# Optimization experiments

Hardware: AMD Instinct MI355X
Metric: run time of the kernel (lower is better)

The kernel has to match this reference:

```python
import jax, jax.numpy as jnp
import numpy as np

N_RAYS = 131072
N_SAMPLES = 128
FEAT_DIM = 3
FAR_DELTA = 1e10  # sentinel delta appended for the last sample, as in the torch code


def setup_inputs() -> dict:
    key = jax.random.key(0)
    k1, k2, k3 = jax.random.split(key, 3)
    # densities are non-negative (output of e.g. relu/softplus in NeRF)
    density = jax.random.uniform(k1, (N_RAYS, N_SAMPLES), dtype=jnp.float32) * 2.0
    feature = jax.random.uniform(k2, (N_RAYS, N_SAMPLES, FEAT_DIM), dtype=jnp.float32)
    # monotonically increasing per-ray sample depths: near + cumsum(uniform bins)
    bins = jax.random.uniform(k3, (N_RAYS, N_SAMPLES), dtype=jnp.float32) * 0.05 + 0.01
    depth_values = 1.0 + jnp.cumsum(bins, axis=1)
    return {"density": density, "feature": feature, "depth_values": depth_values}


def reference(density, feature, depth_values):
    # deltas: consecutive depth differences, with a huge last delta (torch.cat(..., 1e10*ones))
    deltas = jnp.concatenate(
        [depth_values[:, 1:] - depth_values[:, :-1],
         jnp.full_like(depth_values[:, :1], FAR_DELTA)],
        axis=-1,
    )  # [N, S]
    att = jnp.exp(-density * deltas)              # exp(-sigma_i * delta_i), [N, S]
    # inclusive prefix product, matching the loop: T[i] = T[i-1]*exp(-sigma_i*delta_i)
    T = jnp.cumprod(att, axis=1)                  # [N, S]
    weights = T * (1.0 - att)                     # [N, S]
    feat_out = jnp.einsum("ns,nsc->nc", weights, feature)      # [N, 3]
    depth_out = jnp.sum(weights * depth_values, axis=1)         # [N]
    return feat_out, depth_out
```

## Files before the change

kernel.cpp:

```cpp
#include <hip/hip_runtime.h>

#define N_RAYS    131072
#define N_SAMPLES 128
#define FAR_DELTA 1e10f

#define THREADS_PER_RAY 8
#define SPT (N_SAMPLES / THREADS_PER_RAY)

__global__ __launch_bounds__(256) void VolumeRenderer_57612691308835_kernel(
    const float* __restrict__ density,
    const float* __restrict__ feature,
    const float* __restrict__ depth,
    float* __restrict__ out_feat,
    float* __restrict__ out_depth)
{
    const int gtid = blockIdx.x * 256 + threadIdx.x;
    const int ray  = gtid >> 3;
    const int sub  = gtid & 7;

    const long sbase = (long)ray * N_SAMPLES + sub * SPT;
    const float4* __restrict__ dp4 = (const float4*)(depth   + sbase);
    const float4* __restrict__ dn4 = (const float4*)(density + sbase);
    const float4* __restrict__ ft4 = (const float4*)(feature + sbase * 3);

    float dep[SPT + 1], den[SPT], f[SPT * 3];
    #pragma unroll
    for (int g = 0; g < SPT / 4; ++g) {
        const float4 v = dp4[g];
        dep[4*g+0] = v.x; dep[4*g+1] = v.y; dep[4*g+2] = v.z; dep[4*g+3] = v.w;
    }
    #pragma unroll
    for (int g = 0; g < SPT / 4; ++g) {
        const float4 v = dn4[g];
        den[4*g+0] = v.x; den[4*g+1] = v.y; den[4*g+2] = v.z; den[4*g+3] = v.w;
    }
    #pragma unroll
    for (int g = 0; g < SPT * 3 / 4; ++g) {
        const float4 v = ft4[g];
        f[4*g+0] = v.x; f[4*g+1] = v.y; f[4*g+2] = v.z; f[4*g+3] = v.w;
    }

    dep[SPT] = __shfl_down(dep[0], 1);

    float Tloc = 1.0f;
    float sfx = 0.f, sfy = 0.f, sfz = 0.f, sdd = 0.f;
    #pragma unroll
    for (int i = 0; i < SPT; ++i) {
        const float delta = (sub == 7 && i == SPT - 1) ? FAR_DELTA
                                                       : (dep[i + 1] - dep[i]);
        const float att = __expf(-den[i] * delta);
        Tloc *= att;
        const float w = Tloc * (1.0f - att);
        sfx += w * f[3*i + 0];
        sfy += w * f[3*i + 1];
        sfz += w * f[3*i + 2];
        sdd += w * dep[i];
    }

    float p = Tloc, v;
    v = __shfl_up(p, 1); if (sub >= 1) p *= v;
    v = __shfl_up(p, 2); if (sub >= 2) p *= v;
    v = __shfl_up(p, 4); if (sub >= 4) p *= v;
    float excl = __shfl_up(p, 1);
    if (sub == 0) excl = 1.0f;

    sfx *= excl; sfy *= excl; sfz *= excl; sdd *= excl;

    #pragma unroll
    for (int off = 1; off <= 4; off <<= 1) {
        sfx += __shfl_xor(sfx, off);
        sfy += __shfl_xor(sfy, off);
        sfz += __shfl_xor(sfz, off);
        sdd += __shfl_xor(sdd, off);
    }

    if (sub == 0) {
        out_feat[ray * 3 + 0] = sfx;
        out_feat[ray * 3 + 1] = sfy;
        out_feat[ray * 3 + 2] = sfz;
        out_depth[ray]        = sdd;
    }
}

extern "C" void kernel_launch(void* const* d_in, const int* in_sizes, int n_in,
                              void* d_out, int out_size, void* d_ws, size_t ws_size,
                              hipStream_t stream) {
    const float* density = (const float*)d_in[0];
    const float* feature = (const float*)d_in[1];
    const float* depth   = (const float*)d_in[2];

    float* out_feat  = (float*)d_out;
    float* out_depth = (float*)d_out + (long)N_RAYS * 3;

    const int total_threads = N_RAYS * THREADS_PER_RAY;
    const int grid = total_threads / 256;
    VolumeRenderer_57612691308835_kernel<<<grid, 256, 0, stream>>>(
        density, feature, depth, out_feat, out_depth);
}
```

Baseline: 372.9 us.

## Stage loads through padded LDS for fully coalesced global reads, 16 threads per ray

Each block now loads its rays' density, depth and feature data with fully coalesced float4 reads, where consecutive threads touch consecutive addresses. The data is staged in padded shared memory to avoid bank conflicts, and each thread then reads back its own sample slice. Threads per ray go from 8 to 16, which adds one more step to the shuffle scan and the reduction. The feature data reuses the same LDS buffer in a second phase, so the kernel now needs extra barriers and holds more registers for the prefetched values.

```diff
diff --git a/kernel.cpp b/kernel.cpp
--- a/kernel.cpp
+++ b/kernel.cpp
@@ -4,8 +4,19 @@
 #define N_SAMPLES 128
 #define FAR_DELTA 1e10f
 
-#define THREADS_PER_RAY 8
-#define SPT (N_SAMPLES / THREADS_PER_RAY)
+#define TPB 256
+#define TPR 16
+#define SPT (N_SAMPLES / TPR)
+#define RPB (TPB / TPR)
+
+#define LDS_WORDS (20 * 384 + 16)
+
+__device__ __forceinline__ int lds_addr(int chunk, int j) {
+    return 20 * chunk + j;
+}
+__device__ __forceinline__ int lds_addr_w(int chunk_base, int W) {
+    return lds_addr(chunk_base + (W >> 4), W & 15);
+}
 
 __global__ __launch_bounds__(256) void VolumeRenderer_57612691308835_kernel(
     const float* __restrict__ density,
@@ -14,60 +25,95 @@
     float* __restrict__ out_feat,
     float* __restrict__ out_depth)
 {
-    const int gtid = blockIdx.x * 256 + threadIdx.x;
-    const int ray  = gtid >> 3;
-    const int sub  = gtid & 7;
+    __shared__ float lds[LDS_WORDS];
 
-    const long sbase = (long)ray * N_SAMPLES + sub * SPT;
-    const float4* __restrict__ dp4 = (const float4*)(depth   + sbase);
-    const float4* __restrict__ dn4 = (const float4*)(density + sbase);
-    const float4* __restrict__ ft4 = (const float4*)(feature + sbase * 3);
+    const int tid = threadIdx.x;
+    const int r   = tid >> 4;
+    const int sub = tid & 15;
+    const int blockRay0 = blockIdx.x * RPB;
 
-    float dep[SPT + 1], den[SPT], f[SPT * 3];
+    const float4* gden = (const float4*)(density + (long)blockRay0 * N_SAMPLES);
+    const float4* gdep = (const float4*)(depth   + (long)blockRay0 * N_SAMPLES);
+    const float4* gft  = (const float4*)(feature + (long)blockRay0 * N_SAMPLES * 3);
+    float4 ld_den[2], ld_dep[2], ld_ft[6];
     #pragma unroll
-    for (int g = 0; g < SPT / 4; ++g) {
-        const float4 v = dp4[g];
-        dep[4*g+0] = v.x; dep[4*g+1] = v.y; dep[4*g+2] = v.z; dep[4*g+3] = v.w;
+    for (int s = 0; s < 2; ++s) ld_den[s] = gden[tid + s * 256];
+    #pragma unroll
+    for (int s = 0; s < 2; ++s) ld_dep[s] = gdep[tid + s * 256];
+    #pragma unroll
+    for (int s = 0; s < 6; ++s) ld_ft[s]  = gft[tid + s * 256];
+
+    #pragma unroll
+    for (int s = 0; s < 2; ++s) {
+        const int W = s * 1024 + 4 * tid;
+        *(float4*)&lds[lds_addr_w(0,   W)] = ld_den[s];
+        *(float4*)&lds[lds_addr_w(128, W)] = ld_dep[s];
     }
-    #pragma unroll
-    for (int g = 0; g < SPT / 4; ++g) {
-        const float4 v = dn4[g];
-        den[4*g+0] = v.x; den[4*g+1] = v.y; den[4*g+2] = v.z; den[4*g+3] = v.w;
+    __syncthreads();
+
+    float den[SPT], dep[SPT];
+    {
+        const int cA = 8 * r + (sub >> 1);
+        const int j0 = 8 * (sub & 1);
+        #pragma unroll
+        for (int h = 0; h < 2; ++h) {
+            const float4 v = *(const float4*)&lds[lds_addr(cA,       j0 + 4 * h)];
+            const float4 w = *(const float4*)&lds[lds_addr(128 + cA, j0 + 4 * h)];
+            den[4*h+0] = v.x; den[4*h+1] = v.y; den[4*h+2] = v.z; den[4*h+3] = v.w;
+            dep[4*h+0] = w.x; dep[4*h+1] = w.y; dep[4*h+2] = w.z; dep[4*h+3] = w.w;
+        }
     }
-    #pragma unroll
-    for (int g = 0; g < SPT * 3 / 4; ++g) {
-        const float4 v = ft4[g];
-        f[4*g+0] = v.x; f[4*g+1] = v.y; f[4*g+2] = v.z; f[4*g+3] = v.w;
-    }
+    const float next_dep = __shfl_down(dep[0], 1);
 
-    dep[SPT] = __shfl_down(dep[0], 1);
-
-    float Tloc = 1.0f;
-    float sfx = 0.f, sfy = 0.f, sfz = 0.f, sdd = 0.f;
+    float w8[SPT];
+    float Tloc = 1.0f, sdd = 0.f;
     #pragma unroll
     for (int i = 0; i < SPT; ++i) {
-        const float delta = (sub == 7 && i == SPT - 1) ? FAR_DELTA
-                                                       : (dep[i + 1] - dep[i]);
-        const float att = __expf(-den[i] * delta);
+        const float dnext = (i < SPT - 1) ? dep[i + 1]
+                          : (sub == TPR - 1 ? dep[i] + FAR_DELTA : next_dep);
+        const float att = __expf(-den[i] * (dnext - dep[i]));
         Tloc *= att;
-        const float w = Tloc * (1.0f - att);
-        sfx += w * f[3*i + 0];
-        sfy += w * f[3*i + 1];
-        sfz += w * f[3*i + 2];
-        sdd += w * dep[i];
+        w8[i] = Tloc * (1.0f - att);
+        sdd += w8[i] * dep[i];
     }
 
     float p = Tloc, v;
     v = __shfl_up(p, 1); if (sub >= 1) p *= v;
     v = __shfl_up(p, 2); if (sub >= 2) p *= v;
     v = __shfl_up(p, 4); if (sub >= 4) p *= v;
+    v = __shfl_up(p, 8); if (sub >= 8) p *= v;
     float excl = __shfl_up(p, 1);
     if (sub == 0) excl = 1.0f;
 
-    sfx *= excl; sfy *= excl; sfz *= excl; sdd *= excl;
+    __syncthreads();
 
     #pragma unroll
-    for (int off = 1; off <= 4; off <<= 1) {
+    for (int s = 0; s < 6; ++s) {
+        const int W = s * 1024 + 4 * tid;
+        *(float4*)&lds[lds_addr_w(0, W)] = ld_ft[s];
+    }
+    __syncthreads();
+
+    float sfx = 0.f, sfy = 0.f, sfz = 0.f;
+    {
+        const int Wbase = r * 384 + 24 * sub;
+        float f[24];
+        #pragma unroll
+        for (int k = 0; k < 6; ++k) {
+            const float4 q = *(const float4*)&lds[lds_addr_w(0, Wbase + 4 * k)];
+            f[4*k+0] = q.x; f[4*k+1] = q.y; f[4*k+2] = q.z; f[4*k+3] = q.w;
+        }
+        #pragma unroll
+        for (int i = 0; i < SPT; ++i) {
+            sfx += w8[i] * f[3*i + 0];
+            sfy += w8[i] * f[3*i + 1];
+            sfz += w8[i] * f[3*i + 2];
+        }
+    }
+
+    sfx *= excl; sfy *= excl; sfz *= excl; sdd *= excl;
+    #pragma unroll
+    for (int off = 1; off <= 8; off <<= 1) {
         sfx += __shfl_xor(sfx, off);
         sfy += __shfl_xor(sfy, off);
         sfz += __shfl_xor(sfz, off);
@@ -75,6 +121,7 @@
     }
 
     if (sub == 0) {
+        const int ray = blockRay0 + r;
         out_feat[ray * 3 + 0] = sfx;
         out_feat[ray * 3 + 1] = sfy;
         out_feat[ray * 3 + 2] = sfz;
@@ -92,8 +139,7 @@
     float* out_feat  = (float*)d_out;
     float* out_depth = (float*)d_out + (long)N_RAYS * 3;
 
-    const int total_threads = N_RAYS * THREADS_PER_RAY;
-    const int grid = total_threads / 256;
-    VolumeRenderer_57612691308835_kernel<<<grid, 256, 0, stream>>>(
+    const int grid = N_RAYS / RPB;
+    VolumeRenderer_57612691308835_kernel<<<grid, TPB, 0, stream>>>(
         density, feature, depth, out_feat, out_depth);
 }
```

Result: no change. 371.5 us (-0.4%).
